# Kernel tuning notes

Hardware: AMD Instinct MI355X
Metric: run time of the kernel (lower is better)

## Reference

```python
import jax, jax.numpy as jnp
import numpy as np

N_NODES = 50000

def setup_inputs() -> dict:
    key = jax.random.key(0)
    k1, k2, k3, k4, k5, k6 = jax.random.split(key, 6)
    N, E, D_IN, D_OUT = N_NODES, 800000, 128, 128
    feature = jax.random.normal(k1, (N, D_IN), dtype=jnp.float32)
    src = jax.random.randint(k2, (E,), 0, N, dtype=jnp.int64)
    dst = jax.random.randint(k3, (E,), 0, N, dtype=jnp.int64)
    w = jax.random.uniform(k4, (E,), dtype=jnp.float32)
    W = jax.random.normal(k5, (D_OUT, D_IN), dtype=jnp.float32) * (1.0 / np.sqrt(D_IN))
    b = jax.random.normal(k6, (D_OUT,), dtype=jnp.float32) * 0.01
    return {"feature": feature, "src": src, "dst": dst, "w": w, "W": W, "b": b}

def reference(feature, src, dst, w, W, b):
    # gcn_msg: gather source node features, scale by per-edge weight  [E, D]
    msg = feature[src] * w[:, None]
    # fn.sum: scatter-sum messages into destination nodes  [N, D]
    agg = jax.ops.segment_sum(msg, dst, num_segments=N_NODES)
    # NodeApplyModule: linear + activation
    h = agg @ W.T + b
    return jax.nn.relu(h)
```

## Files before the change

### kernel.cpp

```cpp
#include <hip/hip_runtime.h>

#define D 128
#define TILE_M 64
#define BS_STRIDE 129
#define AS_STRIDE 68
#define WS_STRIDE 136
#define DS_STRIDE 136
#define GEMM_BLOCKS 768
#define CAP 64
#define CSH 9
#define CBCAP 16384
#define P1_BLOCKS 256
#define P1_CHUNK_MAX 3200

typedef __attribute__((ext_vector_type(8))) short short8;
typedef __attribute__((ext_vector_type(4))) float floatx4;
typedef __attribute__((ext_vector_type(4))) unsigned short ushortx4;

__device__ __forceinline__ unsigned short f2bf(float f) {
    unsigned u = __float_as_uint(f);
    u += 0x7fffu + ((u >> 16) & 1u);
    return (unsigned short)(u >> 16);
}

__global__ __launch_bounds__(256) void edge_partition(
    const int* __restrict__ src, const int* __restrict__ dst,
    const float* __restrict__ w, int* __restrict__ gcnt,
    uint2* __restrict__ binned, int N, int E)
{
    __shared__ int hist[128], startb[128], cursor[128], gbase[128];
    __shared__ uint2 grouped[P1_CHUNK_MAX];
    const int tid = threadIdx.x;
    const int ncb = (N + 511) >> CSH;
    const int chunk = (E + P1_BLOCKS - 1) / P1_BLOCKS;
    const int base = blockIdx.x * chunk;
    const int lim = (E - base) < chunk ? (E - base) : chunk;

    if (tid < 128) hist[tid] = 0;
    __syncthreads();
    for (int i = tid; i < lim; i += 256)
        atomicAdd(&hist[dst[base + i] >> CSH], 1);
    __syncthreads();
    if (tid == 0) {
        int s = 0;
        for (int b = 0; b < ncb; ++b) { startb[b] = s; s += hist[b]; }
    }
    __syncthreads();
    if (tid < ncb) {
        gbase[tid]  = atomicAdd(&gcnt[tid], hist[tid]);
        cursor[tid] = startb[tid];
    }
    __syncthreads();
    for (int i = tid; i < lim; i += 256) {
        int e = base + i;
        int d = dst[e];
        unsigned rec = ((unsigned)f2bf(w[e]) << 16) | (unsigned)src[e];
        int g = atomicAdd(&cursor[d >> CSH], 1);
        grouped[g] = make_uint2((unsigned)d, rec);
    }
    __syncthreads();
    for (int i = tid; i < lim; i += 256) {
        uint2 v = grouped[i];
        int b = (int)(v.x >> CSH);
        int off = gbase[b] + (i - startb[b]);
        if (off < CBCAP)
            binned[(size_t)b * CBCAP + (size_t)off] = v;
    }
}

__global__ __launch_bounds__(256) void csr_from_bins(
    const uint2* __restrict__ binned, const int* __restrict__ gcnt,
    unsigned* __restrict__ ep, int* __restrict__ cnt, int N)
{
    __shared__ unsigned rowsT[CAP * 128];
    __shared__ int lcnt[128];
    __shared__ int maxc;
    const int tid = threadIdx.x;
    const int fb = blockIdx.x;
    const int d0 = fb << 7;
    const int cb = fb >> 2;

    if (tid < 128) lcnt[tid] = 0;
    __syncthreads();
    int len = gcnt[cb];
    len = len < CBCAP ? len : CBCAP;
    const uint2* bp = binned + (size_t)cb * CBCAP;
    for (int i = tid; i < len; i += 256) {
        uint2 v = bp[i];
        int d = (int)v.x;
        if ((d >> 7) == fb) {
            int pos = atomicAdd(&lcnt[d & 127], 1);
            if (pos < CAP) rowsT[pos * 128 + (d & 127)] = v.y;
        }
    }
    __syncthreads();
    if (tid == 0) {
        int m = 0;
        for (int j = 0; j < 128; ++j) m = m > lcnt[j] ? m : lcnt[j];
        maxc = m < CAP ? m : CAP;
    }
    __syncthreads();
    const int pu = maxc;
    for (int idx = tid; idx < (pu << 7); idx += 256) {
        int p = idx >> 7, j = idx & 127;
        int d = d0 + j;
        if (d < N) ep[(size_t)p * N + d] = rowsT[idx];
    }
    if (tid < 128) {
        int d = d0 + tid;
        if (d < N) cnt[d] = lcnt[tid];
    }
}

__global__ __launch_bounds__(256) void gemm_tf(
    const float* __restrict__ feat, const float* __restrict__ Wm,
    unsigned short* __restrict__ tf, int N)
{
    __shared__ unsigned short Ws[128 * WS_STRIDE];
    __shared__ unsigned short Ds[64 * DS_STRIDE];

    const int tid = threadIdx.x;
    for (int idx = tid; idx < 128 * 128 / 4; idx += 256) {
        int r = idx >> 5;
        int c = (idx & 31) * 4;
        const float4 v = reinterpret_cast<const float4*>(Wm)[idx];
        ushortx4 s;
        s[0] = f2bf(v.x); s[1] = f2bf(v.y); s[2] = f2bf(v.z); s[3] = f2bf(v.w);
        *reinterpret_cast<ushortx4*>(&Ws[r * WS_STRIDE + c]) = s;
    }
    __syncthreads();

    const int lane = tid & 63;
    const int wave = tid >> 6;
    const int kq = (lane >> 4) * 8;
    const int ntiles = (N + 63) >> 6;

    for (int t = blockIdx.x; t < ntiles; t += GEMM_BLOCKS) {
        const int node0 = t * 64;
        const int mr = node0 + wave * 16 + (lane & 15);
        const float* arow = feat + (size_t)(mr < N ? mr : (N - 1)) * D + kq;

        short8 a[4];
#pragma unroll
        for (int kt = 0; kt < 4; ++kt) {
            const float* p = arow + kt * 32;
            const float4 lo = *reinterpret_cast<const float4*>(p);
            const float4 hi = *reinterpret_cast<const float4*>(p + 4);
            short8 v;
            v[0] = (short)f2bf(lo.x); v[1] = (short)f2bf(lo.y);
            v[2] = (short)f2bf(lo.z); v[3] = (short)f2bf(lo.w);
            v[4] = (short)f2bf(hi.x); v[5] = (short)f2bf(hi.y);
            v[6] = (short)f2bf(hi.z); v[7] = (short)f2bf(hi.w);
            a[kt] = v;
        }

        floatx4 acc[8];
#pragma unroll
        for (int nt = 0; nt < 8; ++nt) {
            acc[nt][0] = 0.f; acc[nt][1] = 0.f; acc[nt][2] = 0.f; acc[nt][3] = 0.f;
        }
#pragma unroll
        for (int nt = 0; nt < 8; ++nt) {
            const unsigned short* brow = &Ws[(nt * 16 + (lane & 15)) * WS_STRIDE + kq];
#pragma unroll
            for (int kt = 0; kt < 4; ++kt) {
                short8 b = *reinterpret_cast<const short8*>(brow + kt * 32);
                acc[nt] = __builtin_amdgcn_mfma_f32_16x16x32_bf16(a[kt], b, acc[nt], 0, 0, 0);
            }
        }

        __syncthreads();
        const int mlocal = wave * 16 + (lane >> 4) * 4;
        const int col = lane & 15;
#pragma unroll
        for (int r = 0; r < 4; ++r) {
            unsigned short* drow = &Ds[(mlocal + r) * DS_STRIDE + col];
#pragma unroll
            for (int nt = 0; nt < 8; ++nt)
                drow[nt * 16] = f2bf(acc[nt][r]);
        }
        __syncthreads();

        for (int idx = tid; idx < 64 * 16; idx += 256) {
            int row = idx >> 4;
            int chunk = idx & 15;
            int m = node0 + row;
            if (m < N) {
                uint4 v = *reinterpret_cast<const uint4*>(&Ds[row * DS_STRIDE + chunk * 8]);
                *reinterpret_cast<uint4*>(tf + (size_t)m * D + chunk * 8) = v;
            }
        }
    }
}

__global__ __launch_bounds__(256) void csr_gather_bf16(
    const unsigned short* __restrict__ tf, const unsigned* __restrict__ ep,
    const int* __restrict__ cnt, const float* __restrict__ bias,
    float* __restrict__ out, int N)
{
    int node = blockIdx.x * 16 + (threadIdx.x >> 4);
    if (node >= N) return;
    const int lane = threadIdx.x & 15;
    const int c = lane << 3;
    const unsigned* col = ep + node;
    int end = cnt[node];
    end = end < CAP ? end : CAP;
    int p = 0;
    float a0 = 0.f, a1 = 0.f, a2 = 0.f, a3 = 0.f;
    float a4 = 0.f, a5 = 0.f, a6 = 0.f, a7 = 0.f;

#define ACC8(Q, W)                                       \
    a0 += __uint_as_float((Q).x << 16) * (W);            \
    a1 += __uint_as_float((Q).x & 0xffff0000u) * (W);    \
    a2 += __uint_as_float((Q).y << 16) * (W);            \
    a3 += __uint_as_float((Q).y & 0xffff0000u) * (W);    \
    a4 += __uint_as_float((Q).z << 16) * (W);            \
    a5 += __uint_as_float((Q).z & 0xffff0000u) * (W);    \
    a6 += __uint_as_float((Q).w << 16) * (W);            \
    a7 += __uint_as_float((Q).w & 0xffff0000u) * (W);

    for (; p + 7 < end; p += 8) {
        unsigned r[8];
#pragma unroll
        for (int j = 0; j < 8; ++j) r[j] = col[(size_t)(p + j) * N];
        uint4 q[8];
        float wv[8];
#pragma unroll
        for (int j = 0; j < 8; ++j) {
            q[j] = *reinterpret_cast<const uint4*>(tf + (size_t)(r[j] & 0xffffu) * D + c);
            wv[j] = __uint_as_float(r[j] & 0xffff0000u);
        }
#pragma unroll
        for (int j = 0; j < 8; ++j) { ACC8(q[j], wv[j]) }
    }
    for (; p + 3 < end; p += 4) {
        unsigned r[4];
#pragma unroll
        for (int j = 0; j < 4; ++j) r[j] = col[(size_t)(p + j) * N];
        uint4 q[4];
        float wv[4];
#pragma unroll
        for (int j = 0; j < 4; ++j) {
            q[j] = *reinterpret_cast<const uint4*>(tf + (size_t)(r[j] & 0xffffu) * D + c);
            wv[j] = __uint_as_float(r[j] & 0xffff0000u);
        }
#pragma unroll
        for (int j = 0; j < 4; ++j) { ACC8(q[j], wv[j]) }
    }
    for (; p < end; ++p) {
        unsigned r = col[(size_t)p * N];
        float wv = __uint_as_float(r & 0xffff0000u);
        uint4 q = *reinterpret_cast<const uint4*>(tf + (size_t)(r & 0xffffu) * D + c);
        ACC8(q, wv)
    }
#undef ACC8

    const float4 bv0 = *reinterpret_cast<const float4*>(bias + c);
    const float4 bv1 = *reinterpret_cast<const float4*>(bias + c + 4);
    float4 r0, r1;
    r0.x = fmaxf(a0 + bv0.x, 0.f);
    r0.y = fmaxf(a1 + bv0.y, 0.f);
    r0.z = fmaxf(a2 + bv0.z, 0.f);
    r0.w = fmaxf(a3 + bv0.w, 0.f);
    r1.x = fmaxf(a4 + bv1.x, 0.f);
    r1.y = fmaxf(a5 + bv1.y, 0.f);
    r1.z = fmaxf(a6 + bv1.z, 0.f);
    r1.w = fmaxf(a7 + bv1.w, 0.f);
    float* o = out + (size_t)node * D + c;
    *reinterpret_cast<float4*>(o) = r0;
    *reinterpret_cast<float4*>(o + 4) = r1;
}

__global__ __launch_bounds__(256) void edge_scatter(
    const float* __restrict__ feat, const int* __restrict__ src,
    const int* __restrict__ dst, const float* __restrict__ w,
    float* __restrict__ agg, int E)
{
    long long idx = (long long)blockIdx.x * 256 + threadIdx.x;
    int e = (int)(idx >> 5);
    if (e >= E) return;
    int c = ((int)idx & 31) << 2;
    int s = src[e];
    int d = dst[e];
    float wv = w[e];
    const float4 f = *reinterpret_cast<const float4*>(feat + (size_t)s * D + c);
    float* a = agg + (size_t)d * D + c;
    atomicAdd(a + 0, f.x * wv);
    atomicAdd(a + 1, f.y * wv);
    atomicAdd(a + 2, f.z * wv);
    atomicAdd(a + 3, f.w * wv);
}

__global__ __launch_bounds__(256) void node_linear(
    const float* __restrict__ in, const float* __restrict__ Wm,
    const float* __restrict__ bias, float* __restrict__ out, int N)
{
    __shared__ float Bs[64 * BS_STRIDE];
    __shared__ float As[TILE_M * AS_STRIDE];
    const int tid = threadIdx.x;
    const int tx = tid & 15;
    const int ty = tid >> 4;
    const int node0 = blockIdx.x * TILE_M;
    float acc[4][8];
#pragma unroll
    for (int i = 0; i < 4; ++i)
#pragma unroll
        for (int jj = 0; jj < 8; ++jj) acc[i][jj] = 0.0f;
    for (int kh = 0; kh < 2; ++kh) {
        const int kbase = kh * 64;
        for (int i = tid; i < 128 * 64; i += 256) {
            int j = i >> 6, k = i & 63;
            Bs[k * BS_STRIDE + j] = Wm[j * 128 + kbase + k];
        }
        for (int i = tid; i < TILE_M * 64; i += 256) {
            int m = i >> 6, k = i & 63;
            int n = node0 + m;
            As[m * AS_STRIDE + k] = (n < N) ? in[(size_t)n * D + kbase + k] : 0.0f;
        }
        __syncthreads();
        for (int k0 = 0; k0 < 64; k0 += 4) {
            float a[4][4];
#pragma unroll
            for (int i = 0; i < 4; ++i) {
                const float4 v = *reinterpret_cast<const float4*>(&As[(ty * 4 + i) * AS_STRIDE + k0]);
                a[i][0] = v.x; a[i][1] = v.y; a[i][2] = v.z; a[i][3] = v.w;
            }
#pragma unroll
            for (int kk = 0; kk < 4; ++kk) {
                float bv[8];
#pragma unroll
                for (int jj = 0; jj < 8; ++jj) bv[jj] = Bs[(k0 + kk) * BS_STRIDE + tx + 16 * jj];
#pragma unroll
                for (int i = 0; i < 4; ++i)
#pragma unroll
                    for (int jj = 0; jj < 8; ++jj) acc[i][jj] += a[i][kk] * bv[jj];
            }
        }
        __syncthreads();
    }
    float bv[8];
#pragma unroll
    for (int jj = 0; jj < 8; ++jj) bv[jj] = bias[tx + 16 * jj];
#pragma unroll
    for (int i = 0; i < 4; ++i) {
        int n = node0 + ty * 4 + i;
        if (n < N) {
            float* o = out + (size_t)n * D;
#pragma unroll
            for (int jj = 0; jj < 8; ++jj) {
                float v = acc[i][jj] + bv[jj];
                o[tx + 16 * jj] = v > 0.0f ? v : 0.0f;
            }
        }
    }
}

extern "C" void kernel_launch(void* const* d_in, const int* in_sizes, int n_in,
                              void* d_out, int out_size, void* d_ws, size_t ws_size,
                              hipStream_t stream) {
    const float* feat = (const float*)d_in[0];
    const int*   src  = (const int*)d_in[1];
    const int*   dst  = (const int*)d_in[2];
    const float* w    = (const float*)d_in[3];
    const float* Wm   = (const float*)d_in[4];
    const float* bias = (const float*)d_in[5];
    float* out = (float*)d_out;

    const int N = in_sizes[0] / D;
    const int E = in_sizes[1];

    const int ncb = (N + 511) >> CSH;
    const int nfb = (N + 127) >> 7;

    const size_t ep_b     = (size_t)N * CAP * 4;
    const size_t cnt_b    = (size_t)N * sizeof(int);
    const size_t tf_b     = (size_t)N * D * 2;
    const size_t binned_b = (size_t)ncb * CBCAP * sizeof(uint2);
    const size_t gcnt_b   = 128 * sizeof(int);
    auto align_up = [](size_t x) { return (x + 255) & ~(size_t)255; };

    const size_t need_full = align_up(ep_b) + align_up(cnt_b) + align_up(tf_b) +
                             align_up(binned_b) + align_up(gcnt_b);

    if (ws_size >= need_full && N <= 65536 &&
        E <= P1_BLOCKS * P1_CHUNK_MAX &&
        (long long)E <= (long long)N * (CAP / 4)) {
        char* p = (char*)d_ws;
        unsigned* ep     = (unsigned*)p;       p += align_up(ep_b);
        int*      cnt    = (int*)p;            p += align_up(cnt_b);
        unsigned short* tf = (unsigned short*)p; p += align_up(tf_b);
        uint2*    binned = (uint2*)p;          p += align_up(binned_b);
        int*      gcnt   = (int*)p;

        (void)hipMemsetAsync(gcnt, 0, gcnt_b, stream);
        edge_partition<<<P1_BLOCKS, 256, 0, stream>>>(src, dst, w, gcnt, binned, N, E);
        csr_from_bins<<<nfb, 256, 0, stream>>>(binned, gcnt, ep, cnt, N);
        gemm_tf<<<GEMM_BLOCKS, 256, 0, stream>>>(feat, Wm, tf, N);
        csr_gather_bf16<<<(N + 15) / 16, 256, 0, stream>>>(tf, ep, cnt, bias, out, N);
    } else {
        (void)hipMemsetAsync(out, 0, (size_t)N * D * sizeof(float), stream);
        long long st = (long long)E * 32;
        edge_scatter<<<(int)((st + 255) / 256), 256, 0, stream>>>(feat, src, dst, w, out, E);
        node_linear<<<(N + TILE_M - 1) / TILE_M, 256, 0, stream>>>(out, Wm, bias, out, N);
    }
}
```

Measured before the change: 160.7 us.

## Merge CSR build and feature GEMM into one launch, vectorize edge partition

Merges the CSR-from-bins kernel and the bf16 feature GEMM into a single launch, with blocks split by index: the first nfb blocks build CSR rows and the rest run the GEMM. The two independent stages can then run concurrently and one launch gap goes away. The edge partition now uses 512 blocks with a fixed chunk size and int4/float4 loads, and the bin reads use 16-byte loads. In exchange, the fused kernel reserves shared memory for the larger of the two stages in every block, which may lower occupancy.

```diff
diff --git a/kernel.cpp b/kernel.cpp
--- a/kernel.cpp
+++ b/kernel.cpp
@@ -10,8 +10,8 @@
 #define CAP 64
 #define CSH 9
 #define CBCAP 16384
-#define P1_BLOCKS 256
-#define P1_CHUNK_MAX 3200
+#define P1_BLOCKS 512
+#define P1_CHUNK 1564
 
 typedef __attribute__((ext_vector_type(8))) short short8;
 typedef __attribute__((ext_vector_type(4))) float floatx4;
@@ -29,16 +29,25 @@
     uint2* __restrict__ binned, int N, int E)
 {
     __shared__ int hist[128], startb[128], cursor[128], gbase[128];
-    __shared__ uint2 grouped[P1_CHUNK_MAX];
+    __shared__ uint2 grouped[P1_CHUNK];
     const int tid = threadIdx.x;
     const int ncb = (N + 511) >> CSH;
-    const int chunk = (E + P1_BLOCKS - 1) / P1_BLOCKS;
-    const int base = blockIdx.x * chunk;
-    const int lim = (E - base) < chunk ? (E - base) : chunk;
+    const int base = blockIdx.x * P1_CHUNK;
+    int lim = E - base;
+    if (lim > P1_CHUNK) lim = P1_CHUNK;
+    if (lim < 0) lim = 0;
+    const int lim4 = lim & ~3;
 
     if (tid < 128) hist[tid] = 0;
     __syncthreads();
-    for (int i = tid; i < lim; i += 256)
+    for (int i = tid * 4; i < lim4; i += 1024) {
+        const int4 d4 = *reinterpret_cast<const int4*>(dst + base + i);
+        atomicAdd(&hist[d4.x >> CSH], 1);
+        atomicAdd(&hist[d4.y >> CSH], 1);
+        atomicAdd(&hist[d4.z >> CSH], 1);
+        atomicAdd(&hist[d4.w >> CSH], 1);
+    }
+    for (int i = lim4 + tid; i < lim; i += 256)
         atomicAdd(&hist[dst[base + i] >> CSH], 1);
     __syncthreads();
     if (tid == 0) {
@@ -51,7 +60,21 @@
         cursor[tid] = startb[tid];
     }
     __syncthreads();
-    for (int i = tid; i < lim; i += 256) {
+    for (int i = tid * 4; i < lim4; i += 1024) {
+        const int4   d4 = *reinterpret_cast<const int4*>(dst + base + i);
+        const int4   s4 = *reinterpret_cast<const int4*>(src + base + i);
+        const float4 w4 = *reinterpret_cast<const float4*>(w + base + i);
+#pragma unroll
+        for (int j = 0; j < 4; ++j) {
+            int   d  = (j == 0) ? d4.x : (j == 1) ? d4.y : (j == 2) ? d4.z : d4.w;
+            int   sj = (j == 0) ? s4.x : (j == 1) ? s4.y : (j == 2) ? s4.z : s4.w;
+            float wj = (j == 0) ? w4.x : (j == 1) ? w4.y : (j == 2) ? w4.z : w4.w;
+            unsigned rec = ((unsigned)f2bf(wj) << 16) | (unsigned)sj;
+            int g = atomicAdd(&cursor[d >> CSH], 1);
+            grouped[g] = make_uint2((unsigned)d, rec);
+        }
+    }
+    for (int i = lim4 + tid; i < lim; i += 256) {
         int e = base + i;
         int d = dst[e];
         unsigned rec = ((unsigned)f2bf(w[e]) << 16) | (unsigned)src[e];
@@ -68,58 +91,74 @@
     }
 }
 
-__global__ __launch_bounds__(256) void csr_from_bins(
+__global__ __launch_bounds__(256) void csr_gemm(
     const uint2* __restrict__ binned, const int* __restrict__ gcnt,
-    unsigned* __restrict__ ep, int* __restrict__ cnt, int N)
-{
-    __shared__ unsigned rowsT[CAP * 128];
-    __shared__ int lcnt[128];
-    __shared__ int maxc;
-    const int tid = threadIdx.x;
-    const int fb = blockIdx.x;
-    const int d0 = fb << 7;
-    const int cb = fb >> 2;
-
-    if (tid < 128) lcnt[tid] = 0;
-    __syncthreads();
-    int len = gcnt[cb];
-    len = len < CBCAP ? len : CBCAP;
-    const uint2* bp = binned + (size_t)cb * CBCAP;
-    for (int i = tid; i < len; i += 256) {
-        uint2 v = bp[i];
-        int d = (int)v.x;
-        if ((d >> 7) == fb) {
-            int pos = atomicAdd(&lcnt[d & 127], 1);
-            if (pos < CAP) rowsT[pos * 128 + (d & 127)] = v.y;
-        }
-    }
-    __syncthreads();
-    if (tid == 0) {
-        int m = 0;
-        for (int j = 0; j < 128; ++j) m = m > lcnt[j] ? m : lcnt[j];
-        maxc = m < CAP ? m : CAP;
-    }
-    __syncthreads();
-    const int pu = maxc;
-    for (int idx = tid; idx < (pu << 7); idx += 256) {
-        int p = idx >> 7, j = idx & 127;
-        int d = d0 + j;
-        if (d < N) ep[(size_t)p * N + d] = rowsT[idx];
-    }
-    if (tid < 128) {
-        int d = d0 + tid;
-        if (d < N) cnt[d] = lcnt[tid];
-    }
-}
-
-__global__ __launch_bounds__(256) void gemm_tf(
+    unsigned* __restrict__ ep, int* __restrict__ cnt,
     const float* __restrict__ feat, const float* __restrict__ Wm,
     unsigned short* __restrict__ tf, int N)
 {
-    __shared__ unsigned short Ws[128 * WS_STRIDE];
-    __shared__ unsigned short Ds[64 * DS_STRIDE];
-
+    __shared__ char smem[52224] __attribute__((aligned(16)));
     const int tid = threadIdx.x;
+    const int nfb = (N + 127) >> 7;
+
+    if ((int)blockIdx.x < nfb) {
+        unsigned* rowsT = reinterpret_cast<unsigned*>(smem);
+        int* lcnt       = reinterpret_cast<int*>(smem + 32768);
+        int* maxcp      = reinterpret_cast<int*>(smem + 32768 + 512);
+        const int fb = blockIdx.x;
+        const int d0 = fb << 7;
+        const int cb = fb >> 2;
+
+        if (tid < 128) lcnt[tid] = 0;
+        __syncthreads();
+        int len = gcnt[cb];
+        len = len < CBCAP ? len : CBCAP;
+        const uint2* bp = binned + (size_t)cb * CBCAP;
+        const int len2 = len & ~1;
+        for (int i = tid * 2; i < len2; i += 512) {
+            const uint4 v2 = *reinterpret_cast<const uint4*>(bp + i);
+            int da = (int)v2.x;
+            if ((da >> 7) == fb) {
+                int pos = atomicAdd(&lcnt[da & 127], 1);
+                if (pos < CAP) rowsT[pos * 128 + (da & 127)] = v2.y;
+            }
+            int db = (int)v2.z;
+            if ((db >> 7) == fb) {
+                int pos = atomicAdd(&lcnt[db & 127], 1);
+                if (pos < CAP) rowsT[pos * 128 + (db & 127)] = v2.w;
+            }
+        }
+        for (int i = len2 + tid; i < len; i += 256) {
+            uint2 v = bp[i];
+            int d = (int)v.x;
+            if ((d >> 7) == fb) {
+                int pos = atomicAdd(&lcnt[d & 127], 1);
+                if (pos < CAP) rowsT[pos * 128 + (d & 127)] = v.y;
+            }
+        }
+        __syncthreads();
+        if (tid == 0) {
+            int m = 0;
+            for (int j = 0; j < 128; ++j) m = m > lcnt[j] ? m : lcnt[j];
+            *maxcp = m < CAP ? m : CAP;
+        }
+        __syncthreads();
+        const int pu = *maxcp;
+        for (int idx = tid; idx < (pu << 7); idx += 256) {
+            int p = idx >> 7, j = idx & 127;
+            int d = d0 + j;
+            if (d < N) ep[(size_t)p * N + d] = rowsT[idx];
+        }
+        if (tid < 128) {
+            int d = d0 + tid;
+            if (d < N) cnt[d] = lcnt[tid];
+        }
+        return;
+    }
+
+    unsigned short* Ws = reinterpret_cast<unsigned short*>(smem);
+    unsigned short* Ds = reinterpret_cast<unsigned short*>(smem + 34816);
+
     for (int idx = tid; idx < 128 * 128 / 4; idx += 256) {
         int r = idx >> 5;
         int c = (idx & 31) * 4;
@@ -135,7 +174,7 @@
     const int kq = (lane >> 4) * 8;
     const int ntiles = (N + 63) >> 6;
 
-    for (int t = blockIdx.x; t < ntiles; t += GEMM_BLOCKS) {
+    for (int t = blockIdx.x - nfb; t < ntiles; t += GEMM_BLOCKS) {
         const int node0 = t * 64;
         const int mr = node0 + wave * 16 + (lane & 15);
         const float* arow = feat + (size_t)(mr < N ? mr : (N - 1)) * D + kq;
@@ -383,7 +422,7 @@
                              align_up(binned_b) + align_up(gcnt_b);
 
     if (ws_size >= need_full && N <= 65536 &&
-        E <= P1_BLOCKS * P1_CHUNK_MAX &&
+        E <= P1_BLOCKS * P1_CHUNK &&
         (long long)E <= (long long)N * (CAP / 4)) {
         char* p = (char*)d_ws;
         unsigned* ep     = (unsigned*)p;       p += align_up(ep_b);
@@ -394,8 +433,8 @@
 
         (void)hipMemsetAsync(gcnt, 0, gcnt_b, stream);
         edge_partition<<<P1_BLOCKS, 256, 0, stream>>>(src, dst, w, gcnt, binned, N, E);
-        csr_from_bins<<<nfb, 256, 0, stream>>>(binned, gcnt, ep, cnt, N);
-        gemm_tf<<<GEMM_BLOCKS, 256, 0, stream>>>(feat, Wm, tf, N);
+        csr_gemm<<<nfb + GEMM_BLOCKS, 256, 0, stream>>>(binned, gcnt, ep, cnt,
+                                                        feat, Wm, tf, N);
         csr_gather_bf16<<<(N + 15) / 16, 256, 0, stream>>>(tf, ep, cnt, bias, out, N);
     } else {
         (void)hipMemsetAsync(out, 0, (size_t)N * D * sizeof(float), stream);
```

Measured after the change: 147.5 us. -8.2%, faster.
